# Optimization experiments

Measured on AMD Instinct MI355X. Metric: run time of the kernel, lower is better.

Reference implementation:

```python
import jax, jax.numpy as jnp
import numpy as np

B, C, N_MAX = 32, 1, 1024
HID, CLS, ATT_E, ATT_H = 128, 64, 64, 128
D = HID + CLS            # node_state_dim = hidden + class_repr
EDGE_F = 2 * ATT_E       # 128
K_MIX = 20
N_GNN = B * C * N_MAX    # 32768 GNN nodes
N_FEAT = N_GNN + 1       # node_feat rows after zero-pad row
E = 200_000
E_OUT = 500_000
NUM_SUB = 1024
NUM_PROP = 2             # num_GNN_prop (num_GNN_layers = 1)


def _lin(k, din, dout):
    k1, k2 = jax.random.split(k)
    s = 1.0 / np.sqrt(din)
    return (jax.random.uniform(k1, (din, dout), minval=-s, maxval=s),
            jax.random.uniform(k2, (dout,), minval=-s, maxval=s))


def setup_inputs() -> dict:
    key = jax.random.key(0)
    ks = jax.random.split(key, 30)
    inp = {}
    inp['A_pad'] = (jax.random.uniform(ks[0], (B, C, N_MAX, N_MAX)) < 0.05).astype(jnp.float32)
    inp['edges'] = jax.random.randint(ks[1], (E, 2), 0, N_GNN)
    inp['att_idx'] = jax.random.randint(ks[2], (N_GNN,), 0, ATT_E)
    inp['node_idx_feat'] = jax.random.randint(ks[3], (N_GNN,), 0, N_FEAT)
    inp['class_label'] = jax.random.randint(ks[4], (N_GNN,), 0, 2)
    inp['node_idx_gnn'] = jax.random.randint(ks[5], (E_OUT, 2), 0, N_GNN)
    inp['label'] = (jax.random.uniform(ks[6], (E_OUT,)) < 0.3).astype(jnp.float32)
    inp['subgraph_idx'] = jax.random.randint(ks[7], (E_OUT,), 0, NUM_SUB)
    # learned parameters
    inp['W_dec'], inp['b_dec'] = _lin(ks[8], N_MAX, HID)
    inp['class_emb'] = jax.random.normal(ks[9], (2, CLS)) * 0.1
    inp['W_msg1'], inp['b_msg1'] = _lin(ks[10], D + EDGE_F, D)
    inp['W_msg2'], inp['b_msg2'] = _lin(ks[11], D, D)
    inp['W_att1'], inp['b_att1'] = _lin(ks[12], D + EDGE_F, ATT_H)
    inp['W_att2'], inp['b_att2'] = _lin(ks[13], ATT_H, D)
    inp['W_ih'], inp['b_ih'] = _lin(ks[14], D, 3 * D)
    inp['W_hh'], inp['b_hh'] = _lin(ks[15], D, 3 * D)
    inp['Wt1'], inp['bt1'] = _lin(ks[16], D, HID)
    inp['Wt2'], inp['bt2'] = _lin(ks[17], HID, HID)
    inp['Wt3'], inp['bt3'] = _lin(ks[18], HID, K_MIX)
    inp['Wa1'], inp['ba1'] = _lin(ks[19], D, HID)
    inp['Wa2'], inp['ba2'] = _lin(ks[20], HID, HID)
    inp['Wa3'], inp['ba3'] = _lin(ks[21], HID, K_MIX)
    return inp


def _gran_forward(A_pad, label, W_dec, b_dec, class_emb,
                  W_msg1, b_msg1, W_msg2, b_msg2, W_att1, b_att1, W_att2, b_att2,
                  W_ih, b_ih, W_hh, b_hh, Wt1, bt1, Wt2, bt2, Wt3, bt3,
                  Wa1, ba1, Wa2, ba2, Wa3, ba3,
                  edges, att_idx, node_idx_feat, class_label, node_idx_gnn, subgraph_idx):
    # decoder_input: (B*C*N_max, N_max) -> hidden, then zero-pad one row on top
    A = A_pad.reshape(B * C * N_MAX, N_MAX)
    node_feat = A @ W_dec + b_dec                                   # [N_GNN, HID]
    node_feat = jnp.concatenate([jnp.zeros((1, HID), node_feat.dtype), node_feat], axis=0)
    # att_edge_feat: one-hot(att_idx[src]) || one-hot(att_idx[dst])  (scatter of ones)
    att_edge_feat = jnp.concatenate([
        jax.nn.one_hot(att_idx[edges[:, 0]], ATT_E, dtype=node_feat.dtype),
        jax.nn.one_hot(att_idx[edges[:, 1]], ATT_E, dtype=node_feat.dtype)], axis=1)  # [E, 128]
    # node state = gathered feat ++ class representation
    state = jnp.concatenate([node_feat[node_idx_feat], class_emb[class_label]], axis=1)  # [N_GNN, D]

    src, dst = edges[:, 0], edges[:, 1]

    def prop(state):
        diff = state[src] - state[dst]                              # gather node-diff [E, D]
        ei = jnp.concatenate([diff, att_edge_feat], axis=1)          # [E, D+128]
        msg = jax.nn.relu(ei @ W_msg1 + b_msg1) @ W_msg2 + b_msg2   # edge MLP [E, D]
        att = jax.nn.sigmoid(jax.nn.relu(ei @ W_att1 + b_att1) @ W_att2 + b_att2)
        agg = jax.ops.segment_sum(msg * att, dst, num_segments=N_GNN)  # scatter-add [N_GNN, D]
        # GRUCell(agg, state)
        gi = agg @ W_ih + b_ih
        gh = state @ W_hh + b_hh
        ir, iz, inn = jnp.split(gi, 3, axis=1)
        hr, hz, hn = jnp.split(gh, 3, axis=1)
        r = jax.nn.sigmoid(ir + hr)
        z = jax.nn.sigmoid(iz + hz)
        n = jnp.tanh(inn + r * hn)
        return (1.0 - z) * n + z * state

    for _ in range(NUM_PROP):
        state = prop(state)

    # output edge predictions from state diffs
    dout = state[node_idx_gnn[:, 0]] - state[node_idx_gnn[:, 1]]    # [E_OUT, D]
    h = jax.nn.relu(jax.nn.relu(dout @ Wt1 + bt1) @ Wt2 + bt2)
    log_theta = h @ Wt3 + bt3                                        # [E_OUT, K]
    g = jax.nn.relu(jax.nn.relu(dout @ Wa1 + ba1) @ Wa2 + ba2)
    log_alpha = jax.nn.log_softmax(g @ Wa3 + ba3, axis=1)            # [E_OUT, K]

    # mixture Bernoulli loss (BCEWithLogits, pos_weight=1): softplus(x) - x*y
    adj_loss = jax.nn.softplus(log_theta) - log_theta * label[:, None]
    const = jax.ops.segment_sum(jnp.ones((E_OUT,), log_theta.dtype), subgraph_idx, num_segments=NUM_SUB)
    const = jnp.maximum(const, 1.0)  # guard empty subgraphs with random indices
    red_loss = jax.ops.segment_sum(adj_loss, subgraph_idx, num_segments=NUM_SUB)
    red_alpha = jax.ops.segment_sum(log_alpha, subgraph_idx, num_segments=NUM_SUB) / const[:, None]
    log_prob = jax.nn.logsumexp(-red_loss + red_alpha, axis=1)       # [NUM_SUB]
    return -jnp.sum(log_prob) / float(E_OUT)


def reference(A_pad, edges, att_idx, node_idx_feat, class_label, node_idx_gnn, label, subgraph_idx,
              W_dec, b_dec, class_emb, W_msg1, b_msg1, W_msg2, b_msg2,
              W_att1, b_att1, W_att2, b_att2, W_ih, b_ih, W_hh, b_hh,
              Wt1, bt1, Wt2, bt2, Wt3, bt3, Wa1, ba1, Wa2, ba2, Wa3, ba3):
    return _gran_forward(A_pad, label, W_dec, b_dec, class_emb,
                         W_msg1, b_msg1, W_msg2, b_msg2, W_att1, b_att1, W_att2, b_att2,
                         W_ih, b_ih, W_hh, b_hh, Wt1, bt1, Wt2, bt2, Wt3, bt3,
                         Wa1, ba1, Wa2, ba2, Wa3, ba3,
                         edges, att_idx, node_idx_feat, class_label, node_idx_gnn, subgraph_idx)
```

## Files before the change

### kernel.cpp

```cpp
#include <hip/hip_runtime.h>
#include <math.h>

#define NGNN   32768
#define NMAXD  1024
#define HIDD   128
#define CLSD   64
#define DDIM   192
#define ATTH   128
#define NEDGE  200000
#define NEOUT  500000
#define NSUB   1024
#define KMIX   20

#define NREP      64
#define LOSS_OFF  0
#define ALPHA_OFF 20480
#define CNT_OFF   40960
#define REP_STRIDE 41984

typedef __attribute__((ext_vector_type(8))) short bf16x8;
typedef __attribute__((ext_vector_type(8))) unsigned short u16x8;
typedef __attribute__((ext_vector_type(4))) float f32x4;

__device__ __forceinline__ float sigm(float x) { return 1.0f / (1.0f + __expf(-x)); }
__device__ __forceinline__ float tanhf_(float x) { return 2.0f / (1.0f + __expf(-2.0f * x)) - 1.0f; }

__device__ __forceinline__ short f2bf(float f) {
  union { float f; unsigned u; } v; v.f = f;
  unsigned r = v.u + 0x7FFFu + ((v.u >> 16) & 1u);
  return (short)(r >> 16);
}
__device__ __forceinline__ float bf2f(unsigned short u) {
  union { unsigned u; float f; } v; v.u = ((unsigned)u) << 16;
  return v.f;
}
__device__ __forceinline__ f32x4 bc4(float b) {
  f32x4 v; v[0] = b; v[1] = b; v[2] = b; v[3] = b; return v;
}

__global__ __launch_bounds__(64) void k_pack(const float* __restrict__ W,
                                             short* __restrict__ out, int N, int CT) {
  const int l = threadIdx.x;
  const int ks = blockIdx.x / CT;
  const int ct = blockIdx.x % CT;
  const int row0 = ks * 32 + (l >> 4) * 8;
  const int col = ct * 16 + (l & 15);
  short v[8];
#pragma unroll
  for (int j = 0; j < 8; j++) {
    const float f = (col < N) ? W[(size_t)(row0 + j) * N + col] : 0.0f;
    v[j] = f2bf(f);
  }
  *(bf16x8*)(out + ((size_t)blockIdx.x * 64 + l) * 8) = *(bf16x8*)v;
}

__global__ __launch_bounds__(128) void k_dec(
    const float* __restrict__ A, const float* __restrict__ Wd,
    const float* __restrict__ bd, float* __restrict__ nf) {
  __shared__ float arow[NMAXD];
  __shared__ int   nz[NMAXD];
  __shared__ int   cnt;
  const int row = blockIdx.x;
  const int t = threadIdx.x;
  if (t == 0) cnt = 0;
  const float4* A4 = (const float4*)(A + (size_t)row * NMAXD);
  float4* a4 = (float4*)arow;
  a4[t] = A4[t];
  a4[t + 128] = A4[t + 128];
  __syncthreads();
  for (int i = t; i < NMAXD; i += 128) {
    if (arow[i] != 0.0f) {
      int p = atomicAdd(&cnt, 1);
      nz[p] = i;
    }
  }
  __syncthreads();
  float acc = bd[t];
  const int n = cnt;
  for (int i = 0; i < n; i++) acc += Wd[(size_t)nz[i] * HIDD + t];
  nf[(size_t)row * HIDD + t] = acc;
}

__global__ __launch_bounds__(192) void k_state(
    const float* __restrict__ nf, const float* __restrict__ cemb,
    const int* __restrict__ nif, const int* __restrict__ cl,
    unsigned short* __restrict__ stbf) {
  const int i = blockIdx.x;
  const int t = threadIdx.x;
  float v;
  if (t < HIDD) {
    const int idx = nif[i];
    v = (idx == 0) ? 0.0f : nf[(size_t)(idx - 1) * HIDD + t];
  } else {
    v = cemb[cl[i] * CLSD + (t - HIDD)];
  }
  stbf[(size_t)i * DDIM + t] = (unsigned short)f2bf(v);
}

__global__ __launch_bounds__(128, 4) void k_edge_mfma(
    const unsigned short* __restrict__ stbf, const int* __restrict__ edges,
    const int* __restrict__ attidx,
    const float* __restrict__ Wm1, const float* __restrict__ bm1,
    const short* __restrict__ pWm1, const short* __restrict__ pWm2,
    const float* __restrict__ bm2,
    const float* __restrict__ Wa1, const float* __restrict__ ba1,
    const short* __restrict__ pWa1, const short* __restrict__ pWa2,
    const float* __restrict__ ba2,
    float* __restrict__ agg) {
  __shared__ short phm[6144];
  __shared__ short pha[4096];
  const int t = threadIdx.x;
  const int e0 = blockIdx.x * 32;
  const int wid = t >> 6, l = t & 63;
  const int col16 = l & 15, rr = (l >> 4) * 4;
  const int cb = (l >> 4) * 8;

  bf16x8 dfrag[6];
  {
    const int e = e0 + wid * 16 + (l & 15);
    const int s = edges[2 * e], d = edges[2 * e + 1];
    const unsigned short* ps = &stbf[(size_t)s * DDIM + cb];
    const unsigned short* pd_ = &stbf[(size_t)d * DDIM + cb];
#pragma unroll
    for (int ks = 0; ks < 6; ks++) {
      const u16x8 a = *(const u16x8*)(ps + ks * 32);
      const u16x8 b = *(const u16x8*)(pd_ + ks * 32);
      short v[8];
#pragma unroll
      for (int j = 0; j < 8; j++) v[j] = f2bf(bf2f(a[j]) - bf2f(b[j]));
      dfrag[ks] = *(bf16x8*)v;
    }
  }
  int a0r[4], a1r[4], dstr[4];
#pragma unroll
  for (int j = 0; j < 4; j++) {
    const int e = e0 + wid * 16 + rr + j;
    const int s = edges[2 * e], d = edges[2 * e + 1];
    a0r[j] = attidx[s]; a1r[j] = attidx[d]; dstr[j] = d;
  }

  for (int ct = 0; ct < 12; ct++) {
    const int col = ct * 16 + col16;
    f32x4 acc;
#pragma unroll
    for (int j = 0; j < 4; j++)
      acc[j] = bm1[col] + Wm1[(size_t)(DDIM + a0r[j]) * DDIM + col]
                        + Wm1[(size_t)(DDIM + 64 + a1r[j]) * DDIM + col];
#pragma unroll
    for (int ks = 0; ks < 6; ks++) {
      bf16x8 b = *(const bf16x8*)&pWm1[((ks * 12 + ct) * 64 + l) * 8];
      acc = __builtin_amdgcn_mfma_f32_16x16x32_bf16(dfrag[ks], b, acc, 0, 0, 0);
    }
    const int ksp = col >> 5, gp = (col & 31) >> 3, jp = col & 7;
#pragma unroll
    for (int j = 0; j < 4; j++)
      phm[((wid * 6 + ksp) * 64 + gp * 16 + rr + j) * 8 + jp] = f2bf(fmaxf(acc[j], 0.0f));
  }
  for (int ct = 0; ct < 8; ct++) {
    const int col = ct * 16 + col16;
    f32x4 acc;
#pragma unroll
    for (int j = 0; j < 4; j++)
      acc[j] = ba1[col] + Wa1[(size_t)(DDIM + a0r[j]) * ATTH + col]
                        + Wa1[(size_t)(DDIM + 64 + a1r[j]) * ATTH + col];
#pragma unroll
    for (int ks = 0; ks < 6; ks++) {
      bf16x8 b = *(const bf16x8*)&pWa1[((ks * 8 + ct) * 64 + l) * 8];
      acc = __builtin_amdgcn_mfma_f32_16x16x32_bf16(dfrag[ks], b, acc, 0, 0, 0);
    }
    const int ksp = ct >> 1, gp = ((ct & 1) * 16 + col16) >> 3, jp = col16 & 7;
#pragma unroll
    for (int j = 0; j < 4; j++)
      pha[((wid * 4 + ksp) * 64 + gp * 16 + rr + j) * 8 + jp] = f2bf(fmaxf(acc[j], 0.0f));
  }
  __syncthreads();

  for (int ct = 0; ct < 12; ct++) {
    const int col = ct * 16 + col16;
    f32x4 m = bc4(bm2[col]), av = bc4(ba2[col]);
#pragma unroll
    for (int ks = 0; ks < 6; ks++) {
      bf16x8 a = *(const bf16x8*)&phm[((wid * 6 + ks) * 64 + l) * 8];
      bf16x8 b = *(const bf16x8*)&pWm2[((ks * 12 + ct) * 64 + l) * 8];
      m = __builtin_amdgcn_mfma_f32_16x16x32_bf16(a, b, m, 0, 0, 0);
    }
#pragma unroll
    for (int ks = 0; ks < 4; ks++) {
      bf16x8 a = *(const bf16x8*)&pha[((wid * 4 + ks) * 64 + l) * 8];
      bf16x8 b = *(const bf16x8*)&pWa2[((ks * 12 + ct) * 64 + l) * 8];
      av = __builtin_amdgcn_mfma_f32_16x16x32_bf16(a, b, av, 0, 0, 0);
    }
#pragma unroll
    for (int j = 0; j < 4; j++) {
      atomicAdd(&agg[(size_t)dstr[j] * DDIM + col], m[j] * sigm(av[j]));
    }
  }
}

__global__ __launch_bounds__(256, 2) void k_gru_mfma(
    unsigned short* __restrict__ stbf, const float* __restrict__ agg,
    const short* __restrict__ pWih, const float* __restrict__ bih,
    const short* __restrict__ pWhh, const float* __restrict__ bhh) {
  const int t = threadIdx.x;
  const int n0 = blockIdx.x * 64;
  const int wid = t >> 6, l = t & 63;
  const int col16 = l & 15, rr = (l >> 4) * 4;
  const int cb = (l >> 4) * 8;
  const int row = n0 + wid * 16 + (l & 15);

  bf16x8 af[6], sf[6];
#pragma unroll
  for (int ks = 0; ks < 6; ks++) {
    const float4 a0 = *(const float4*)&agg[(size_t)row * DDIM + ks * 32 + cb];
    const float4 a1 = *(const float4*)&agg[(size_t)row * DDIM + ks * 32 + cb + 4];
    short v[8];
    v[0] = f2bf(a0.x); v[1] = f2bf(a0.y); v[2] = f2bf(a0.z); v[3] = f2bf(a0.w);
    v[4] = f2bf(a1.x); v[5] = f2bf(a1.y); v[6] = f2bf(a1.z); v[7] = f2bf(a1.w);
    af[ks] = *(bf16x8*)v;
    sf[ks] = *(const bf16x8*)&stbf[(size_t)row * DDIM + ks * 32 + cb];
  }

  for (int ct = 0; ct < 12; ct++) {
    const int c = ct * 16 + col16;
    f32x4 ir = bc4(bih[c]), iz = bc4(bih[c + DDIM]), in_ = bc4(bih[c + 2 * DDIM]);
    f32x4 hr = bc4(bhh[c]), hz = bc4(bhh[c + DDIM]), hn = bc4(bhh[c + 2 * DDIM]);
#pragma unroll
    for (int ks = 0; ks < 6; ks++) {
      const bf16x8 wr = *(const bf16x8*)&pWih[((size_t)(ks * 36 + ct) * 64 + l) * 8];
      const bf16x8 wz = *(const bf16x8*)&pWih[((size_t)(ks * 36 + ct + 12) * 64 + l) * 8];
      const bf16x8 wn = *(const bf16x8*)&pWih[((size_t)(ks * 36 + ct + 24) * 64 + l) * 8];
      ir  = __builtin_amdgcn_mfma_f32_16x16x32_bf16(af[ks], wr, ir, 0, 0, 0);
      iz  = __builtin_amdgcn_mfma_f32_16x16x32_bf16(af[ks], wz, iz, 0, 0, 0);
      in_ = __builtin_amdgcn_mfma_f32_16x16x32_bf16(af[ks], wn, in_, 0, 0, 0);
      const bf16x8 vr = *(const bf16x8*)&pWhh[((size_t)(ks * 36 + ct) * 64 + l) * 8];
      const bf16x8 vz = *(const bf16x8*)&pWhh[((size_t)(ks * 36 + ct + 12) * 64 + l) * 8];
      const bf16x8 vn = *(const bf16x8*)&pWhh[((size_t)(ks * 36 + ct + 24) * 64 + l) * 8];
      hr = __builtin_amdgcn_mfma_f32_16x16x32_bf16(sf[ks], vr, hr, 0, 0, 0);
      hz = __builtin_amdgcn_mfma_f32_16x16x32_bf16(sf[ks], vz, hz, 0, 0, 0);
      hn = __builtin_amdgcn_mfma_f32_16x16x32_bf16(sf[ks], vn, hn, 0, 0, 0);
    }
#pragma unroll
    for (int j = 0; j < 4; j++) {
      const size_t idx = (size_t)(n0 + wid * 16 + rr + j) * DDIM + c;
      const float sv = bf2f(stbf[idx]);
      const float r = sigm(ir[j] + hr[j]);
      const float z = sigm(iz[j] + hz[j]);
      const float nn = tanhf_(in_[j] + r * hn[j]);
      stbf[idx] = (unsigned short)f2bf((1.0f - z) * nn + z * sv);
    }
  }
}

__global__ __launch_bounds__(512, 2) void k_head_mfma(
    const unsigned short* __restrict__ stbf, const int* __restrict__ nig,
    const float* __restrict__ label, const int* __restrict__ subidx,
    const short* __restrict__ pWt1, const float* __restrict__ bt1,
    const short* __restrict__ pWt2, const float* __restrict__ bt2,
    const short* __restrict__ pWt3, const float* __restrict__ bt3,
    const short* __restrict__ pWa1, const float* __restrict__ ba1,
    const short* __restrict__ pWa2, const float* __restrict__ ba2,
    const short* __restrict__ pWa3, const float* __restrict__ ba3,
    float* __restrict__ REP) {
  __shared__ short ph1t[8192], ph1a[8192];
  __shared__ short ph2t[8192], ph2a[8192];
  __shared__ float la[64 * KMIX];
  __shared__ int   ssub[64];
  __shared__ float slab[64];
  __shared__ float lse[64];

  const int t = threadIdx.x;
  const int r0 = blockIdx.x * 64;
  float* rep = REP + (size_t)(blockIdx.x & (NREP - 1)) * REP_STRIDE;

  if (t < 64) {
    const int gr = r0 + t;
    const int sb = (gr < NEOUT) ? subidx[gr] : 0;
    ssub[t] = sb;
    slab[t] = (gr < NEOUT) ? label[gr] : 0.0f;
    if (gr < NEOUT) atomicAdd(&rep[CNT_OFF + sb], 1.0f);
  }

  const int wid = t >> 6, l = t & 63;
  const int rt = wid & 3, ch = wid >> 2;
  const int col16 = l & 15, rr = (l >> 4) * 4;
  const int cb = (l >> 4) * 8;

  bf16x8 dfrag[6];
  {
    const int gr = r0 + rt * 16 + (l & 15);
    const int ok = (gr < NEOUT);
    const int ia = ok ? nig[2 * gr] : 0;
    const int ib = ok ? nig[2 * gr + 1] : 0;
    const unsigned short* pa = &stbf[(size_t)ia * DDIM + cb];
    const unsigned short* pb = &stbf[(size_t)ib * DDIM + cb];
#pragma unroll
    for (int ks = 0; ks < 6; ks++) {
      const u16x8 a = *(const u16x8*)(pa + ks * 32);
      const u16x8 b = *(const u16x8*)(pb + ks * 32);
      short v[8];
#pragma unroll
      for (int j = 0; j < 8; j++) v[j] = f2bf(bf2f(a[j]) - bf2f(b[j]));
      dfrag[ks] = *(bf16x8*)v;
    }
  }

  for (int ci = 0; ci < 4; ci++) {
    const int ct = ch * 4 + ci;
    const int col = ct * 16 + col16;
    f32x4 at = bc4(bt1[col]), aa = bc4(ba1[col]);
#pragma unroll
    for (int ks = 0; ks < 6; ks++) {
      bf16x8 b1 = *(const bf16x8*)&pWt1[((ks * 8 + ct) * 64 + l) * 8];
      bf16x8 b2 = *(const bf16x8*)&pWa1[((ks * 8 + ct) * 64 + l) * 8];
      at = __builtin_amdgcn_mfma_f32_16x16x32_bf16(dfrag[ks], b1, at, 0, 0, 0);
      aa = __builtin_amdgcn_mfma_f32_16x16x32_bf16(dfrag[ks], b2, aa, 0, 0, 0);
    }
    const int ksp = ct >> 1, gp = ((ct & 1) * 16 + col16) >> 3, jp = col16 & 7;
#pragma unroll
    for (int j = 0; j < 4; j++) {
      const int o = ((rt * 4 + ksp) * 64 + gp * 16 + rr + j) * 8 + jp;
      ph1t[o] = f2bf(fmaxf(at[j], 0.0f));
      ph1a[o] = f2bf(fmaxf(aa[j], 0.0f));
    }
  }
  __syncthreads();
  for (int ci = 0; ci < 4; ci++) {
    const int ct = ch * 4 + ci;
    const int col = ct * 16 + col16;
    f32x4 at = bc4(bt2[col]), aa = bc4(ba2[col]);
#pragma unroll
    for (int ks = 0; ks < 4; ks++) {
      const int ao = ((rt * 4 + ks) * 64 + l) * 8;
      bf16x8 a1 = *(const bf16x8*)&ph1t[ao];
      bf16x8 a2 = *(const bf16x8*)&ph1a[ao];
      bf16x8 b1 = *(const bf16x8*)&pWt2[((ks * 8 + ct) * 64 + l) * 8];
      bf16x8 b2 = *(const bf16x8*)&pWa2[((ks * 8 + ct) * 64 + l) * 8];
      at = __builtin_amdgcn_mfma_f32_16x16x32_bf16(a1, b1, at, 0, 0, 0);
      aa = __builtin_amdgcn_mfma_f32_16x16x32_bf16(a2, b2, aa, 0, 0, 0);
    }
    const int ksp = ct >> 1, gp = ((ct & 1) * 16 + col16) >> 3, jp = col16 & 7;
#pragma unroll
    for (int j = 0; j < 4; j++) {
      const int o = ((rt * 4 + ksp) * 64 + gp * 16 + rr + j) * 8 + jp;
      ph2t[o] = f2bf(fmaxf(at[j], 0.0f));
      ph2a[o] = f2bf(fmaxf(aa[j], 0.0f));
    }
  }
  __syncthreads();
  const int col = ch * 16 + col16;
  f32x4 ot = bc4((col < KMIX) ? bt3[col] : 0.0f);
  f32x4 oa = bc4((col < KMIX) ? ba3[col] : 0.0f);
#pragma unroll
  for (int ks = 0; ks < 4; ks++) {
    const int ao = ((rt * 4 + ks) * 64 + l) * 8;
    bf16x8 a1 = *(const bf16x8*)&ph2t[ao];
    bf16x8 a2 = *(const bf16x8*)&ph2a[ao];
    bf16x8 b1 = *(const bf16x8*)&pWt3[((ks * 2 + ch) * 64 + l) * 8];
    bf16x8 b2 = *(const bf16x8*)&pWa3[((ks * 2 + ch) * 64 + l) * 8];
    ot = __builtin_amdgcn_mfma_f32_16x16x32_bf16(a1, b1, ot, 0, 0, 0);
    oa = __builtin_amdgcn_mfma_f32_16x16x32_bf16(a2, b2, oa, 0, 0, 0);
  }

  if (col < KMIX) {
#pragma unroll
    for (int j = 0; j < 4; j++) {
      const int r = rt * 16 + rr + j;
      if (r0 + r < NEOUT) {
        const float lt = ot[j];
        const float adj = fmaxf(lt, 0.0f) + logf(1.0f + __expf(-fabsf(lt))) - lt * slab[r];
        atomicAdd(&rep[LOSS_OFF + ssub[r] * KMIX + col], adj);
      }
      la[(rt * 16 + rr + j) * KMIX + col] = oa[j];
    }
  }
  __syncthreads();
  if (t < 64) {
    float m = -1e30f;
    for (int k = 0; k < KMIX; k++) m = fmaxf(m, la[t * KMIX + k]);
    float s = 0.0f;
    for (int k = 0; k < KMIX; k++) s += __expf(la[t * KMIX + k] - m);
    lse[t] = m + logf(s);
  }
  __syncthreads();
  {
    const int r = t >> 3;
    if (r0 + r < NEOUT) {
#pragma unroll
      for (int i = 0; i < 3; i++) {
        const int c = (t & 7) + 8 * i;
        if (c < KMIX)
          atomicAdd(&rep[ALPHA_OFF + ssub[r] * KMIX + c], la[r * KMIX + c] - lse[r]);
      }
    }
  }
}

__global__ __launch_bounds__(256) void k_red(const float* __restrict__ REP,
                                             float* __restrict__ fin) {
  const int i = blockIdx.x * 256 + threadIdx.x;
  if (i < REP_STRIDE) {
    float s = 0.0f;
    for (int r = 0; r < NREP; r++) s += REP[(size_t)r * REP_STRIDE + i];
    fin[i] = s;
  }
}

__global__ __launch_bounds__(1024) void k_final(
    const float* __restrict__ fin, float* __restrict__ out) {
  __shared__ float part[1024];
  const int s = threadIdx.x;
  const float* red_loss  = fin + LOSS_OFF;
  const float* red_alpha = fin + ALPHA_OFF;
  const float c = fmaxf(fin[CNT_OFF + s], 1.0f);
  float v[KMIX];
  float m = -1e30f;
  for (int k = 0; k < KMIX; k++) {
    v[k] = -red_loss[s * KMIX + k] + red_alpha[s * KMIX + k] / c;
    m = fmaxf(m, v[k]);
  }
  float sum = 0.0f;
  for (int k = 0; k < KMIX; k++) sum += __expf(v[k] - m);
  part[s] = m + logf(sum);
  __syncthreads();
  for (int st = 512; st > 0; st >>= 1) {
    if (s < st) part[s] += part[s + st];
    __syncthreads();
  }
  if (s == 0) out[0] = -part[0] / (float)NEOUT;
}

extern "C" void kernel_launch(void* const* d_in, const int* in_sizes, int n_in,
                              void* d_out, int out_size, void* d_ws, size_t ws_size,
                              hipStream_t stream) {
  const float* A      = (const float*)d_in[0];
  const int*   edges  = (const int*)d_in[1];
  const int*   attidx = (const int*)d_in[2];
  const int*   nif    = (const int*)d_in[3];
  const int*   cl     = (const int*)d_in[4];
  const int*   nig    = (const int*)d_in[5];
  const float* label  = (const float*)d_in[6];
  const int*   subidx = (const int*)d_in[7];
  const float* Wdec   = (const float*)d_in[8];
  const float* bdec   = (const float*)d_in[9];
  const float* cemb   = (const float*)d_in[10];
  const float* Wm1    = (const float*)d_in[11];
  const float* bm1    = (const float*)d_in[12];
  const float* Wm2    = (const float*)d_in[13];
  const float* bm2    = (const float*)d_in[14];
  const float* Wa1    = (const float*)d_in[15];
  const float* ba1    = (const float*)d_in[16];
  const float* Wa2    = (const float*)d_in[17];
  const float* ba2    = (const float*)d_in[18];
  const float* Wih    = (const float*)d_in[19];
  const float* bih    = (const float*)d_in[20];
  const float* Whh    = (const float*)d_in[21];
  const float* bhh    = (const float*)d_in[22];
  const float* Wt1    = (const float*)d_in[23];
  const float* bt1    = (const float*)d_in[24];
  const float* Wt2    = (const float*)d_in[25];
  const float* bt2    = (const float*)d_in[26];
  const float* Wt3    = (const float*)d_in[27];
  const float* bt3    = (const float*)d_in[28];
  const float* Wha1   = (const float*)d_in[29];
  const float* hba1   = (const float*)d_in[30];
  const float* Wha2   = (const float*)d_in[31];
  const float* hba2   = (const float*)d_in[32];
  const float* Wha3   = (const float*)d_in[33];
  const float* hba3   = (const float*)d_in[34];

  char* ws = (char*)d_ws;
  const size_t SZ_STBF = (size_t)NGNN * DDIM * sizeof(short);
  const size_t SZ_AGG  = (size_t)NGNN * DDIM * sizeof(float);
  const size_t SZ_REP  = (size_t)NREP * REP_STRIDE * sizeof(float);
  unsigned short* stbf = (unsigned short*)ws;
  float* agg       = (float*)(ws + SZ_STBF);
  float* nf        = agg;
  float* REP       = (float*)(ws + SZ_STBF + SZ_AGG);
  float* fin       = (float*)(ws + SZ_STBF + SZ_AGG + SZ_REP);
  short* pk        = (short*)(ws + SZ_STBF + SZ_AGG + SZ_REP +
                              (((size_t)REP_STRIDE * 4 + 255) / 256) * 256);
  short* pWm1  = pk;
  short* pWa1e = pWm1  + 36864;
  short* pWm2  = pWa1e + 24576;
  short* pWa2e = pWm2  + 36864;
  short* pWt1  = pWa2e + 24576;
  short* pWt2  = pWt1  + 24576;
  short* pWt3  = pWt2  + 16384;
  short* pWh1  = pWt3  + 4096;
  short* pWh2  = pWh1  + 24576;
  short* pWh3  = pWh2  + 16384;
  short* pWih  = pWh3  + 4096;
  short* pWhh  = pWih  + 110592;

  k_pack<<<72, 64, 0, stream>>>(Wm1,  pWm1,  192, 12);
  k_pack<<<48, 64, 0, stream>>>(Wa1,  pWa1e, 128, 8);
  k_pack<<<72, 64, 0, stream>>>(Wm2,  pWm2,  192, 12);
  k_pack<<<48, 64, 0, stream>>>(Wa2,  pWa2e, 192, 12);
  k_pack<<<48, 64, 0, stream>>>(Wt1,  pWt1,  128, 8);
  k_pack<<<32, 64, 0, stream>>>(Wt2,  pWt2,  128, 8);
  k_pack<<< 8, 64, 0, stream>>>(Wt3,  pWt3,   20, 2);
  k_pack<<<48, 64, 0, stream>>>(Wha1, pWh1,  128, 8);
  k_pack<<<32, 64, 0, stream>>>(Wha2, pWh2,  128, 8);
  k_pack<<< 8, 64, 0, stream>>>(Wha3, pWh3,   20, 2);
  k_pack<<<216, 64, 0, stream>>>(Wih, pWih,  576, 36);
  k_pack<<<216, 64, 0, stream>>>(Whh, pWhh,  576, 36);

  k_dec<<<NGNN, 128, 0, stream>>>(A, Wdec, bdec, nf);
  k_state<<<NGNN, 192, 0, stream>>>(nf, cemb, nif, cl, stbf);
  for (int p = 0; p < 2; p++) {
    hipMemsetAsync(agg, 0, SZ_AGG, stream);
    k_edge_mfma<<<NEDGE / 32, 128, 0, stream>>>(stbf, edges, attidx,
        Wm1, bm1, pWm1, pWm2, bm2, Wa1, ba1, pWa1e, pWa2e, ba2, agg);
    k_gru_mfma<<<NGNN / 64, 256, 0, stream>>>(stbf, agg, pWih, bih, pWhh, bhh);
  }
  hipMemsetAsync(REP, 0, SZ_REP, stream);
  k_head_mfma<<<(NEOUT + 63) / 64, 512, 0, stream>>>(stbf, nig, label, subidx,
      pWt1, bt1, pWt2, bt2, pWt3, bt3, pWh1, hba1, pWh2, hba2, pWh3, hba3, REP);
  k_red<<<(REP_STRIDE + 255) / 256, 256, 0, stream>>>(REP, fin);
  k_final<<<1, 1024, 0, stream>>>(fin, (float*)d_out);
}
```

Baseline: 962.7 us.

## Restructure edge and head MFMA kernels for weight-fragment reuse across row tiles

```diff
diff --git a/kernel.cpp b/kernel.cpp
--- a/kernel.cpp
+++ b/kernel.cpp
@@ -97,7 +97,7 @@
   stbf[(size_t)i * DDIM + t] = (unsigned short)f2bf(v);
 }
 
-__global__ __launch_bounds__(128, 4) void k_edge_mfma(
+__global__ __launch_bounds__(128, 3) void k_edge_mfma(
     const unsigned short* __restrict__ stbf, const int* __restrict__ edges,
     const int* __restrict__ attidx,
     const float* __restrict__ Wm1, const float* __restrict__ bm1,
@@ -107,6 +107,7 @@
     const short* __restrict__ pWa1, const short* __restrict__ pWa2,
     const float* __restrict__ ba2,
     float* __restrict__ agg) {
+  __shared__ short pdiff[6144];
   __shared__ short phm[6144];
   __shared__ short pha[4096];
   const int t = threadIdx.x;
@@ -115,7 +116,7 @@
   const int col16 = l & 15, rr = (l >> 4) * 4;
   const int cb = (l >> 4) * 8;
 
-  bf16x8 dfrag[6];
+  bf16x8 afr[2][6];
   {
     const int e = e0 + wid * 16 + (l & 15);
     const int s = edges[2 * e], d = edges[2 * e + 1];
@@ -128,72 +129,108 @@
       short v[8];
 #pragma unroll
       for (int j = 0; j < 8; j++) v[j] = f2bf(bf2f(a[j]) - bf2f(b[j]));
-      dfrag[ks] = *(bf16x8*)v;
-    }
-  }
-  int a0r[4], a1r[4], dstr[4];
-#pragma unroll
-  for (int j = 0; j < 4; j++) {
-    const int e = e0 + wid * 16 + rr + j;
-    const int s = edges[2 * e], d = edges[2 * e + 1];
-    a0r[j] = attidx[s]; a1r[j] = attidx[d]; dstr[j] = d;
-  }
-
-  for (int ct = 0; ct < 12; ct++) {
+      afr[wid][ks] = *(bf16x8*)v;
+      *(bf16x8*)&pdiff[((wid * 6 + ks) * 64 + l) * 8] = afr[wid][ks];
+    }
+  }
+  int a0r[2][4], a1r[2][4], dstr[2][4];
+#pragma unroll
+  for (int rt = 0; rt < 2; rt++)
+#pragma unroll
+    for (int j = 0; j < 4; j++) {
+      const int e = e0 + rt * 16 + rr + j;
+      const int s = edges[2 * e], d = edges[2 * e + 1];
+      a0r[rt][j] = attidx[s]; a1r[rt][j] = attidx[d]; dstr[rt][j] = d;
+    }
+  __syncthreads();
+  {
+    const int o = wid ^ 1;
+#pragma unroll
+    for (int ks = 0; ks < 6; ks++)
+      afr[o][ks] = *(const bf16x8*)&pdiff[((o * 6 + ks) * 64 + l) * 8];
+  }
+
+  for (int ci = 0; ci < 6; ci++) {
+    const int ct = wid * 6 + ci;
     const int col = ct * 16 + col16;
-    f32x4 acc;
-#pragma unroll
-    for (int j = 0; j < 4; j++)
-      acc[j] = bm1[col] + Wm1[(size_t)(DDIM + a0r[j]) * DDIM + col]
-                        + Wm1[(size_t)(DDIM + 64 + a1r[j]) * DDIM + col];
+    f32x4 acc[2];
+#pragma unroll
+    for (int rt = 0; rt < 2; rt++)
+#pragma unroll
+      for (int j = 0; j < 4; j++)
+        acc[rt][j] = bm1[col] + Wm1[(size_t)(DDIM + a0r[rt][j]) * DDIM + col]
+                              + Wm1[(size_t)(DDIM + 64 + a1r[rt][j]) * DDIM + col];
 #pragma unroll
     for (int ks = 0; ks < 6; ks++) {
-      bf16x8 b = *(const bf16x8*)&pWm1[((ks * 12 + ct) * 64 + l) * 8];
-      acc = __builtin_amdgcn_mfma_f32_16x16x32_bf16(dfrag[ks], b, acc, 0, 0, 0);
+      const bf16x8 b = *(const bf16x8*)&pWm1[((ks * 12 + ct) * 64 + l) * 8];
+      acc[0] = __builtin_amdgcn_mfma_f32_16x16x32_bf16(afr[0][ks], b, acc[0], 0, 0, 0);
+      acc[1] = __builtin_amdgcn_mfma_f32_16x16x32_bf16(afr[1][ks], b, acc[1], 0, 0, 0);
     }
     const int ksp = col >> 5, gp = (col & 31) >> 3, jp = col & 7;
 #pragma unroll
-    for (int j = 0; j < 4; j++)
-      phm[((wid * 6 + ksp) * 64 + gp * 16 + rr + j) * 8 + jp] = f2bf(fmaxf(acc[j], 0.0f));
-  }
-  for (int ct = 0; ct < 8; ct++) {
+    for (int rt = 0; rt < 2; rt++)
+#pragma unroll
+      for (int j = 0; j < 4; j++)
+        phm[((rt * 6 + ksp) * 64 + gp * 16 + rr + j) * 8 + jp] = f2bf(fmaxf(acc[rt][j], 0.0f));
+  }
+  for (int ci = 0; ci < 4; ci++) {
+    const int ct = wid * 4 + ci;
     const int col = ct * 16 + col16;
-    f32x4 acc;
-#pragma unroll
-    for (int j = 0; j < 4; j++)
-      acc[j] = ba1[col] + Wa1[(size_t)(DDIM + a0r[j]) * ATTH + col]
-                        + Wa1[(size_t)(DDIM + 64 + a1r[j]) * ATTH + col];
+    f32x4 acc[2];
+#pragma unroll
+    for (int rt = 0; rt < 2; rt++)
+#pragma unroll
+      for (int j = 0; j < 4; j++)
+        acc[rt][j] = ba1[col] + Wa1[(size_t)(DDIM + a0r[rt][j]) * ATTH + col]
+                              + Wa1[(size_t)(DDIM + 64 + a1r[rt][j]) * ATTH + col];
 #pragma unroll
     for (int ks = 0; ks < 6; ks++) {
-      bf16x8 b = *(const bf16x8*)&pWa1[((ks * 8 + ct) * 64 + l) * 8];
-      acc = __builtin_amdgcn_mfma_f32_16x16x32_bf16(dfrag[ks], b, acc, 0, 0, 0);
-    }
-    const int ksp = ct >> 1, gp = ((ct & 1) * 16 + col16) >> 3, jp = col16 & 7;
-#pragma unroll
-    for (int j = 0; j < 4; j++)
-      pha[((wid * 4 + ksp) * 64 + gp * 16 + rr + j) * 8 + jp] = f2bf(fmaxf(acc[j], 0.0f));
-  }
-  __syncthreads();
-
-  for (int ct = 0; ct < 12; ct++) {
+      const bf16x8 b = *(const bf16x8*)&pWa1[((ks * 8 + ct) * 64 + l) * 8];
+      acc[0] = __builtin_amdgcn_mfma_f32_16x16x32_bf16(afr[0][ks], b, acc[0], 0, 0, 0);
+      acc[1] = __builtin_amdgcn_mfma_f32_16x16x32_bf16(afr[1][ks], b, acc[1], 0, 0, 0);
+    }
+    const int ksp = col >> 5, gp = (col & 31) >> 3, jp = col & 7;
+#pragma unroll
+    for (int rt = 0; rt < 2; rt++)
+#pragma unroll
+      for (int j = 0; j < 4; j++)
+        pha[((rt * 4 + ksp) * 64 + gp * 16 + rr + j) * 8 + jp] = f2bf(fmaxf(acc[rt][j], 0.0f));
+  }
+  __syncthreads();
+
+  bf16x8 hmf[2][6], haf[2][4];
+#pragma unroll
+  for (int rt = 0; rt < 2; rt++) {
+#pragma unroll
+    for (int ks = 0; ks < 6; ks++)
+      hmf[rt][ks] = *(const bf16x8*)&phm[((rt * 6 + ks) * 64 + l) * 8];
+#pragma unroll
+    for (int ks = 0; ks < 4; ks++)
+      haf[rt][ks] = *(const bf16x8*)&pha[((rt * 4 + ks) * 64 + l) * 8];
+  }
+  for (int ci = 0; ci < 6; ci++) {
+    const int ct = wid * 6 + ci;
     const int col = ct * 16 + col16;
-    f32x4 m = bc4(bm2[col]), av = bc4(ba2[col]);
+    f32x4 m[2], av[2];
+    m[0] = bc4(bm2[col]); m[1] = m[0];
+    av[0] = bc4(ba2[col]); av[1] = av[0];
 #pragma unroll
     for (int ks = 0; ks < 6; ks++) {
-      bf16x8 a = *(const bf16x8*)&phm[((wid * 6 + ks) * 64 + l) * 8];
-      bf16x8 b = *(const bf16x8*)&pWm2[((ks * 12 + ct) * 64 + l) * 8];
-      m = __builtin_amdgcn_mfma_f32_16x16x32_bf16(a, b, m, 0, 0, 0);
+      const bf16x8 b = *(const bf16x8*)&pWm2[((ks * 12 + ct) * 64 + l) * 8];
+      m[0] = __builtin_amdgcn_mfma_f32_16x16x32_bf16(hmf[0][ks], b, m[0], 0, 0, 0);
+      m[1] = __builtin_amdgcn_mfma_f32_16x16x32_bf16(hmf[1][ks], b, m[1], 0, 0, 0);
     }
 #pragma unroll
     for (int ks = 0; ks < 4; ks++) {
-      bf16x8 a = *(const bf16x8*)&pha[((wid * 4 + ks) * 64 + l) * 8];
-      bf16x8 b = *(const bf16x8*)&pWa2[((ks * 12 + ct) * 64 + l) * 8];
-      av = __builtin_amdgcn_mfma_f32_16x16x32_bf16(a, b, av, 0, 0, 0);
-    }
-#pragma unroll
-    for (int j = 0; j < 4; j++) {
-      atomicAdd(&agg[(size_t)dstr[j] * DDIM + col], m[j] * sigm(av[j]));
-    }
+      const bf16x8 b = *(const bf16x8*)&pWa2[((ks * 12 + ct) * 64 + l) * 8];
+      av[0] = __builtin_amdgcn_mfma_f32_16x16x32_bf16(haf[0][ks], b, av[0], 0, 0, 0);
+      av[1] = __builtin_amdgcn_mfma_f32_16x16x32_bf16(haf[1][ks], b, av[1], 0, 0, 0);
+    }
+#pragma unroll
+    for (int rt = 0; rt < 2; rt++)
+#pragma unroll
+      for (int j = 0; j < 4; j++)
+        atomicAdd(&agg[(size_t)dstr[rt][j] * DDIM + col], m[rt][j] * sigm(av[rt][j]));
   }
 }
 
@@ -251,7 +288,7 @@
   }
 }
 
-__global__ __launch_bounds__(512, 2) void k_head_mfma(
+__global__ __launch_bounds__(512, 4) void k_head_mfma(
     const unsigned short* __restrict__ stbf, const int* __restrict__ nig,
     const float* __restrict__ label, const int* __restrict__ subidx,
     const short* __restrict__ pWt1, const float* __restrict__ bt1,
@@ -261,8 +298,8 @@
     const short* __restrict__ pWa2, const float* __restrict__ ba2,
     const short* __restrict__ pWa3, const float* __restrict__ ba3,
     float* __restrict__ REP) {
-  __shared__ short ph1t[8192], ph1a[8192];
-  __shared__ short ph2t[8192], ph2a[8192];
+  __shared__ short u1[16384];
+  __shared__ short ph1[16384];
   __shared__ float la[64 * KMIX];
   __shared__ int   ssub[64];
   __shared__ float slab[64];
@@ -280,97 +317,142 @@
     if (gr < NEOUT) atomicAdd(&rep[CNT_OFF + sb], 1.0f);
   }
 
-  const int wid = t >> 6, l = t & 63;
-  const int rt = wid & 3, ch = wid >> 2;
-  const int col16 = l & 15, rr = (l >> 4) * 4;
-  const int cb = (l >> 4) * 8;
-
-  bf16x8 dfrag[6];
-  {
-    const int gr = r0 + rt * 16 + (l & 15);
+  for (int it = 0; it < 3; it++) {
+    const int id = t + 512 * it;
+    const int r = id / 24, g24 = id % 24;
+    const int gr = r0 + r;
     const int ok = (gr < NEOUT);
     const int ia = ok ? nig[2 * gr] : 0;
     const int ib = ok ? nig[2 * gr + 1] : 0;
-    const unsigned short* pa = &stbf[(size_t)ia * DDIM + cb];
-    const unsigned short* pb = &stbf[(size_t)ib * DDIM + cb];
-#pragma unroll
-    for (int ks = 0; ks < 6; ks++) {
-      const u16x8 a = *(const u16x8*)(pa + ks * 32);
-      const u16x8 b = *(const u16x8*)(pb + ks * 32);
-      short v[8];
-#pragma unroll
-      for (int j = 0; j < 8; j++) v[j] = f2bf(bf2f(a[j]) - bf2f(b[j]));
-      dfrag[ks] = *(bf16x8*)v;
-    }
-  }
-
-  for (int ci = 0; ci < 4; ci++) {
-    const int ct = ch * 4 + ci;
-    const int col = ct * 16 + col16;
-    f32x4 at = bc4(bt1[col]), aa = bc4(ba1[col]);
-#pragma unroll
-    for (int ks = 0; ks < 6; ks++) {
-      bf16x8 b1 = *(const bf16x8*)&pWt1[((ks * 8 + ct) * 64 + l) * 8];
-      bf16x8 b2 = *(const bf16x8*)&pWa1[((ks * 8 + ct) * 64 + l) * 8];
-      at = __builtin_amdgcn_mfma_f32_16x16x32_bf16(dfrag[ks], b1, at, 0, 0, 0);
-      aa = __builtin_amdgcn_mfma_f32_16x16x32_bf16(dfrag[ks], b2, aa, 0, 0, 0);
-    }
-    const int ksp = ct >> 1, gp = ((ct & 1) * 16 + col16) >> 3, jp = col16 & 7;
-#pragma unroll
-    for (int j = 0; j < 4; j++) {
-      const int o = ((rt * 4 + ksp) * 64 + gp * 16 + rr + j) * 8 + jp;
-      ph1t[o] = f2bf(fmaxf(at[j], 0.0f));
-      ph1a[o] = f2bf(fmaxf(aa[j], 0.0f));
-    }
-  }
-  __syncthreads();
-  for (int ci = 0; ci < 4; ci++) {
-    const int ct = ch * 4 + ci;
-    const int col = ct * 16 + col16;
-    f32x4 at = bc4(bt2[col]), aa = bc4(ba2[col]);
-#pragma unroll
-    for (int ks = 0; ks < 4; ks++) {
-      const int ao = ((rt * 4 + ks) * 64 + l) * 8;
-      bf16x8 a1 = *(const bf16x8*)&ph1t[ao];
-      bf16x8 a2 = *(const bf16x8*)&ph1a[ao];
-      bf16x8 b1 = *(const bf16x8*)&pWt2[((ks * 8 + ct) * 64 + l) * 8];
-      bf16x8 b2 = *(const bf16x8*)&pWa2[((ks * 8 + ct) * 64 + l) * 8];
-      at = __builtin_amdgcn_mfma_f32_16x16x32_bf16(a1, b1, at, 0, 0, 0);
-      aa = __builtin_amdgcn_mfma_f32_16x16x32_bf16(a2, b2, aa, 0, 0, 0);
-    }
-    const int ksp = ct >> 1, gp = ((ct & 1) * 16 + col16) >> 3, jp = col16 & 7;
-#pragma unroll
-    for (int j = 0; j < 4; j++) {
-      const int o = ((rt * 4 + ksp) * 64 + gp * 16 + rr + j) * 8 + jp;
-      ph2t[o] = f2bf(fmaxf(at[j], 0.0f));
-      ph2a[o] = f2bf(fmaxf(aa[j], 0.0f));
-    }
-  }
-  __syncthreads();
-  const int col = ch * 16 + col16;
-  f32x4 ot = bc4((col < KMIX) ? bt3[col] : 0.0f);
-  f32x4 oa = bc4((col < KMIX) ? ba3[col] : 0.0f);
-#pragma unroll
-  for (int ks = 0; ks < 4; ks++) {
-    const int ao = ((rt * 4 + ks) * 64 + l) * 8;
-    bf16x8 a1 = *(const bf16x8*)&ph2t[ao];
-    bf16x8 a2 = *(const bf16x8*)&ph2a[ao];
-    bf16x8 b1 = *(const bf16x8*)&pWt3[((ks * 2 + ch) * 64 + l) * 8];
-    bf16x8 b2 = *(const bf16x8*)&pWa3[((ks * 2 + ch) * 64 + l) * 8];
-    ot = __builtin_amdgcn_mfma_f32_16x16x32_bf16(a1, b1, ot, 0, 0, 0);
-    oa = __builtin_amdgcn_mfma_f32_16x16x32_bf16(a2, b2, oa, 0, 0, 0);
-  }
-
-  if (col < KMIX) {
-#pragma unroll
-    for (int j = 0; j < 4; j++) {
-      const int r = rt * 16 + rr + j;
-      if (r0 + r < NEOUT) {
-        const float lt = ot[j];
-        const float adj = fmaxf(lt, 0.0f) + logf(1.0f + __expf(-fabsf(lt))) - lt * slab[r];
-        atomicAdd(&rep[LOSS_OFF + ssub[r] * KMIX + col], adj);
+    const u16x8 a = *(const u16x8*)&stbf[(size_t)ia * DDIM + g24 * 8];
+    const u16x8 b = *(const u16x8*)&stbf[(size_t)ib * DDIM + g24 * 8];
+    short v[8];
+#pragma unroll
+    for (int j = 0; j < 8; j++) v[j] = f2bf(bf2f(a[j]) - bf2f(b[j]));
+    const int rt = r >> 4, ks = g24 >> 2, g = g24 & 3;
+    *(bf16x8*)&u1[((rt * 6 + ks) * 64 + g * 16 + (r & 15)) * 8] = *(bf16x8*)v;
+  }
+  __syncthreads();
+
+  const int wid = t >> 6, l = t & 63;
+  const int b = wid >> 2, cw = wid & 3;
+  const int col16 = l & 15, rr = (l >> 4) * 4;
+
+  const short* pW1 = b ? pWa1 : pWt1;
+  const short* pW2 = b ? pWa2 : pWt2;
+  const short* pW3 = b ? pWa3 : pWt3;
+  const float* bv1 = b ? ba1 : bt1;
+  const float* bv2 = b ? ba2 : bt2;
+  const float* bv3 = b ? ba3 : bt3;
+  short* ph1b = ph1 + b * 8192;
+  short* ph2b = u1 + b * 8192;
+
+  {
+    bf16x8 B1[12];
+    float bias[2];
+#pragma unroll
+    for (int c2 = 0; c2 < 2; c2++) {
+      const int ct = cw * 2 + c2;
+      bias[c2] = bv1[ct * 16 + col16];
+#pragma unroll
+      for (int ks = 0; ks < 6; ks++)
+        B1[c2 * 6 + ks] = *(const bf16x8*)&pW1[((ks * 8 + ct) * 64 + l) * 8];
+    }
+    for (int rt = 0; rt < 4; rt++) {
+      bf16x8 a[6];
+#pragma unroll
+      for (int ks = 0; ks < 6; ks++)
+        a[ks] = *(const bf16x8*)&u1[((rt * 6 + ks) * 64 + l) * 8];
+      f32x4 acc0 = bc4(bias[0]), acc1 = bc4(bias[1]);
+#pragma unroll
+      for (int ks = 0; ks < 6; ks++) {
+        acc0 = __builtin_amdgcn_mfma_f32_16x16x32_bf16(a[ks], B1[ks], acc0, 0, 0, 0);
+        acc1 = __builtin_amdgcn_mfma_f32_16x16x32_bf16(a[ks], B1[6 + ks], acc1, 0, 0, 0);
       }
-      la[(rt * 16 + rr + j) * KMIX + col] = oa[j];
+#pragma unroll
+      for (int c2 = 0; c2 < 2; c2++) {
+        const int col = (cw * 2 + c2) * 16 + col16;
+        const int ksp = col >> 5, gp = (col & 31) >> 3, jp = col & 7;
+        const f32x4 acc = c2 ? acc1 : acc0;
+#pragma unroll
+        for (int j = 0; j < 4; j++)
+          ph1b[((rt * 4 + ksp) * 64 + gp * 16 + rr + j) * 8 + jp] = f2bf(fmaxf(acc[j], 0.0f));
+      }
+    }
+  }
+  __syncthreads();
+
+  {
+    bf16x8 B2[8];
+    float bias[2];
+#pragma unroll
+    for (int c2 = 0; c2 < 2; c2++) {
+      const int ct = cw * 2 + c2;
+      bias[c2] = bv2[ct * 16 + col16];
+#pragma unroll
+      for (int ks = 0; ks < 4; ks++)
+        B2[c2 * 4 + ks] = *(const bf16x8*)&pW2[((ks * 8 + ct) * 64 + l) * 8];
+    }
+    for (int rt = 0; rt < 4; rt++) {
+      bf16x8 a[4];
+#pragma unroll
+      for (int ks = 0; ks < 4; ks++)
+        a[ks] = *(const bf16x8*)&ph1b[((rt * 4 + ks) * 64 + l) * 8];
+      f32x4 acc0 = bc4(bias[0]), acc1 = bc4(bias[1]);
+#pragma unroll
+      for (int ks = 0; ks < 4; ks++) {
+        acc0 = __builtin_amdgcn_mfma_f32_16x16x32_bf16(a[ks], B2[ks], acc0, 0, 0, 0);
+        acc1 = __builtin_amdgcn_mfma_f32_16x16x32_bf16(a[ks], B2[4 + ks], acc1, 0, 0, 0);
+      }
+#pragma unroll
+      for (int c2 = 0; c2 < 2; c2++) {
+        const int col = (cw * 2 + c2) * 16 + col16;
+        const int ksp = col >> 5, gp = (col & 31) >> 3, jp = col & 7;
+        const f32x4 acc = c2 ? acc1 : acc0;
+#pragma unroll
+        for (int j = 0; j < 4; j++)
+          ph2b[((rt * 4 + ksp) * 64 + gp * 16 + rr + j) * 8 + jp] = f2bf(fmaxf(acc[j], 0.0f));
+      }
+    }
+  }
+  __syncthreads();
+
+  {
+    const int ct3 = cw & 1, rth = cw >> 1;
+    const int col = ct3 * 16 + col16;
+    bf16x8 B3[4];
+#pragma unroll
+    for (int ks = 0; ks < 4; ks++)
+      B3[ks] = *(const bf16x8*)&pW3[((ks * 2 + ct3) * 64 + l) * 8];
+    const float bias = (col < KMIX) ? bv3[col] : 0.0f;
+#pragma unroll
+    for (int i = 0; i < 2; i++) {
+      const int rt = rth * 2 + i;
+      bf16x8 a[4];
+#pragma unroll
+      for (int ks = 0; ks < 4; ks++)
+        a[ks] = *(const bf16x8*)&ph2b[((rt * 4 + ks) * 64 + l) * 8];
+      f32x4 acc = bc4(bias);
+#pragma unroll
+      for (int ks = 0; ks < 4; ks++)
+        acc = __builtin_amdgcn_mfma_f32_16x16x32_bf16(a[ks], B3[ks], acc, 0, 0, 0);
+      if (col < KMIX) {
+        if (b == 0) {
+#pragma unroll
+          for (int j = 0; j < 4; j++) {
+            const int r = rt * 16 + rr + j;
+            if (r0 + r < NEOUT) {
+              const float lt = acc[j];
+              const float adj = fmaxf(lt, 0.0f) + logf(1.0f + __expf(-fabsf(lt))) - lt * slab[r];
+              atomicAdd(&rep[LOSS_OFF + ssub[r] * KMIX + col], adj);
+            }
+          }
+        } else {
+#pragma unroll
+          for (int j = 0; j < 4; j++)
+            la[(rt * 16 + rr + j) * KMIX + col] = acc[j];
+        }
+      }
     }
   }
   __syncthreads();
```

After: 1.116 ms. 1.16x slower.
